# Kernel tuning notes

Measured on AMD Instinct MI355X. Metric: run time of the kernel, lower is better.

## Reference

```python
import jax, jax.numpy as jnp
import numpy as np

N_NODES = 500_000
N_EDGES = 16_000_000


def _gcn_conv(x, src, dst, deg_inv_sqrt, W, b, n):
    # PyG GCNConv: linear transform, then symmetric-normalized aggregation
    h = x @ W                                   # [N, out]
    norm = deg_inv_sqrt[src] * deg_inv_sqrt[dst]  # [E+N]
    msgs = h[src] * norm[:, None]               # gather + scale, [E+N, out]
    out = jax.ops.segment_sum(msgs, dst, num_segments=n)  # scatter-add
    return out + b


def setup_inputs() -> dict:
    key = jax.random.key(0)
    k1, k2, k3, k4, k5, k6 = jax.random.split(key, 6)
    x = jax.random.normal(k1, (N_NODES, 12), dtype=jnp.float32)
    edge_index = jax.random.randint(k2, (2, N_EDGES), 0, N_NODES, dtype=jnp.int64)
    # glorot-style init for GCNConv weights, zero bias (PyG default)
    W1 = jax.random.normal(k3, (12, 16), dtype=jnp.float32) * (2.0 / (12 + 16)) ** 0.5
    b1 = jnp.zeros((16,), dtype=jnp.float32)
    W2 = jax.random.normal(k4, (16, 8), dtype=jnp.float32) * (2.0 / (16 + 8)) ** 0.5
    b2 = jnp.zeros((8,), dtype=jnp.float32)
    return {"x": x, "edge_index": edge_index, "W1": W1, "b1": b1, "W2": W2, "b2": b2}


def reference(x, edge_index, W1, b1, W2, b2):
    n = x.shape[0]
    # add self-loops (GCNConv default add_self_loops=True)
    loops = jnp.arange(n, dtype=edge_index.dtype)
    src = jnp.concatenate([edge_index[0], loops])
    dst = jnp.concatenate([edge_index[1], loops])
    # symmetric normalization: deg over destination including self-loops
    deg = jax.ops.segment_sum(jnp.ones_like(dst, dtype=x.dtype), dst, num_segments=n)
    deg_inv_sqrt = jnp.where(deg > 0, jax.lax.rsqrt(deg), 0.0)
    h = jax.nn.relu(_gcn_conv(x, src, dst, deg_inv_sqrt, W1, b1, n))
    out = _gcn_conv(h, src, dst, deg_inv_sqrt, W2, b2, n)
    return out
```

## Files before the change

### kernel.cpp

```cpp
#include <hip/hip_runtime.h>

#define TPB 512
#define SCH 8192
#define EPT 16
#define NPB 512
#define NBIN 1024
#define CAP 17408
#define KMAX 34
#define NCHK 16
#define SBIN (NPB * NCHK)
#define PAD1 17
#define PAD2 9

__device__ __forceinline__ unsigned int f2bf(float f) {
    unsigned int u = __float_as_uint(f);
    return (u + 0x7FFFu + ((u >> 16) & 1u)) >> 16;
}
__device__ __forceinline__ float4 bf4(uint2 q) {
    float4 r;
    r.x = __uint_as_float(q.x << 16);
    r.y = __uint_as_float(q.x & 0xFFFF0000u);
    r.z = __uint_as_float(q.y << 16);
    r.w = __uint_as_float(q.y & 0xFFFF0000u);
    return r;
}

__global__ void k_init(int* bcur, int B) {
    int i = blockIdx.x * blockDim.x + threadIdx.x;
    if (i < B) bcur[i] = i * CAP;
}

__global__ void k_scatter(const int* __restrict__ es, const int* __restrict__ ed,
                          int* bcur, int* __restrict__ epk, int E, int B) {
    __shared__ int pay[SCH];
    __shared__ int cnt[NBIN];
    __shared__ int sstart[NBIN + 1];
    __shared__ int gbase[NBIN];
    __shared__ int tsum[TPB];
    int t = threadIdx.x;
    int e0 = blockIdx.x * SCH;
    int m = min(E - e0, SCH);
    for (int i = t; i < NBIN; i += TPB) cnt[i] = 0;
    __syncthreads();
    int pk[EPT], rk[EPT];
#pragma unroll
    for (int k = 0; k < EPT; k++) {
        int i = t + k * TPB;
        if (i < m) {
            int s = es[e0 + i], d = ed[e0 + i];
            int b = d >> 9;
            int r = atomicAdd(&cnt[b], 1);
            rk[k] = (b << 14) | r;
            pk[k] = (s << 9) | (d & (NPB - 1));
        }
    }
    __syncthreads();
    int c0 = cnt[2 * t], c1 = cnt[2 * t + 1];
    tsum[t] = c0 + c1;
    __syncthreads();
    for (int off = 1; off < TPB; off <<= 1) {
        int u = (t >= off) ? tsum[t - off] : 0;
        __syncthreads();
        tsum[t] += u;
        __syncthreads();
    }
    int base = tsum[t] - c0 - c1;
    sstart[2 * t] = base;
    sstart[2 * t + 1] = base + c0;
    if (t == TPB - 1) sstart[NBIN] = tsum[t];
    gbase[2 * t]     = c0 ? atomicAdd(&bcur[2 * t], c0) : 0;
    gbase[2 * t + 1] = c1 ? atomicAdd(&bcur[2 * t + 1], c1) : 0;
    __syncthreads();
#pragma unroll
    for (int k = 0; k < EPT; k++) {
        int i = t + k * TPB;
        if (i < m) pay[sstart[rk[k] >> 14] + (rk[k] & 16383)] = pk[k];
    }
    __syncthreads();
    for (int i = t; i < m; i += TPB) {
        int lo = 0, hi = NBIN;
        while (hi - lo > 1) {
            int mid = (lo + hi) >> 1;
            if (sstart[mid] <= i) lo = mid; else hi = mid;
        }
        epk[gbase[lo] + (i - sstart[lo])] = pay[i];
    }
}

__global__ void k_prepsort(const float* __restrict__ x, const int* __restrict__ bcur,
                           int* epk, const float* __restrict__ W1,
                           float* __restrict__ dis, unsigned int* __restrict__ h0u,
                           int* __restrict__ rowptr, uint4* __restrict__ scnt, int n) {
    __shared__ int cnt[SBIN];
    __shared__ int tsum[TPB];
    __shared__ float sW1[192];
    int t = threadIdx.x;
    int b = blockIdx.x;
    if (t < 192) sW1[t] = W1[t];
    for (int i = t; i < SBIN; i += TPB) cnt[i] = 0;
    __syncthreads();
    int e0 = b * CAP, e1 = bcur[b];
    int p[KMAX];
#pragma unroll
    for (int k = 0; k < KMAX; k++) {
        int idx = e0 + t + k * TPB;
        if (idx < e1) {
            p[k] = epk[idx];
            int bin = ((p[k] & (NPB - 1)) << 4) | ((p[k] >> 24) & 15);
            atomicAdd(&cnt[bin], 1);
        }
    }
    __syncthreads();
    int deg = 0;
#pragma unroll
    for (int j = 0; j < 16; j++) deg += cnt[16 * t + j];
    tsum[t] = deg;
    __syncthreads();
    for (int off = 1; off < TPB; off <<= 1) {
        int u = (t >= off) ? tsum[t - off] : 0;
        __syncthreads();
        tsum[t] += u;
        __syncthreads();
    }
    int run = e0 + tsum[t] - deg;
    int base = b << 9;
    int v = base + t;
    if (v < n) rowptr[v] = run;
    unsigned int cw[4] = {0u, 0u, 0u, 0u};
#pragma unroll
    for (int j = 0; j < 16; j++) {
        int cj = cnt[16 * t + j];
        cnt[16 * t + j] = run;
        run += cj;
        cw[j >> 2] |= ((unsigned int)cj) << ((j & 3) * 8);
    }
    if (v < n) scnt[v] = make_uint4(cw[0], cw[1], cw[2], cw[3]);
    __syncthreads();
    unsigned short* eps = (unsigned short*)epk;
    size_t ebase = (size_t)b * CAP;
#pragma unroll
    for (int k = 0; k < KMAX; k++) {
        int idx = e0 + t + k * TPB;
        if (idx < e1) {
            int bin = ((p[k] & (NPB - 1)) << 4) | ((p[k] >> 24) & 15);
            int pos = atomicAdd(&cnt[bin], 1);
            eps[ebase + pos] = (unsigned short)((p[k] >> 9) & 32767);
        }
    }
    if (v < n) {
        float d = rsqrtf((float)(deg + 1));
        dis[v] = d;
        const float4* xp = (const float4*)(x + (size_t)v * 12);
        float4 a = xp[0], q = xp[1], cc = xp[2];
        float xi[12] = {a.x, a.y, a.z, a.w, q.x, q.y, q.z, q.w, cc.x, cc.y, cc.z, cc.w};
        float o[16];
#pragma unroll
        for (int j = 0; j < 16; j++) {
            float s = 0.f;
#pragma unroll
            for (int k = 0; k < 12; k++) s = fmaf(xi[k], sW1[k * 16 + j], s);
            o[j] = s * d;
        }
        unsigned int w[8];
#pragma unroll
        for (int j = 0; j < 8; j++)
            w[j] = f2bf(o[2 * j]) | (f2bf(o[2 * j + 1]) << 16);
        uint4* hp = (uint4*)(h0u + (size_t)v * 8);
        hp[0] = make_uint4(w[0], w[1], w[2], w[3]);
        hp[1] = make_uint4(w[4], w[5], w[6], w[7]);
    }
}

__global__ void k_agg1(const unsigned int* __restrict__ h0u, const float* __restrict__ dis,
                       const int* __restrict__ rowptr, const int* __restrict__ epk,
                       const unsigned char* __restrict__ scb,
                       const float* __restrict__ b1, const float* __restrict__ W2,
                       unsigned int* __restrict__ h2u, int n) {
    __shared__ float acc[NPB * PAD1];
    __shared__ float sb1[16], sW2[128];
    int t = threadIdx.x;
    int b = blockIdx.x;
    if (t < 128) sW2[t] = W2[t];
    else if (t < 144) sb1[t - 128] = b1[t - 128];
    const unsigned short* eps = ((const unsigned short*)epk) + (size_t)b * CAP;
    const uint2* h0v = (const uint2*)h0u;
    int base = b << 9;
    int nn = min(NPB, n - base);
    int g = t >> 2, m = t & 3;
    float4 a[4];
    int cur[4];
#pragma unroll
    for (int u = 0; u < 4; u++) {
        int vl = 4 * g + u;
        if (vl < nn) {
            int v = base + vl;
            cur[u] = rowptr[v];
            a[u] = bf4(h0v[(size_t)v * 4 + m]);
        } else {
            cur[u] = 0;
            a[u] = make_float4(0.f, 0.f, 0.f, 0.f);
        }
    }
    for (int c = 0; c < NCHK; c++) {
        int cb = c << 15;
#pragma unroll
        for (int u = 0; u < 4; u++) {
            int vl = 4 * g + u;
            if (vl < nn) {
                int cnt = scb[(size_t)(base + vl) * NCHK + c];
                int end = cur[u] + cnt;
                int j = cur[u];
                cur[u] = end;
                for (; j + 1 < end; j += 2) {
                    int s0 = cb | eps[j], s1 = cb | eps[j + 1];
                    float4 q0 = bf4(h0v[(size_t)s0 * 4 + m]);
                    float4 q1 = bf4(h0v[(size_t)s1 * 4 + m]);
                    a[u].x += q0.x + q1.x; a[u].y += q0.y + q1.y;
                    a[u].z += q0.z + q1.z; a[u].w += q0.w + q1.w;
                }
                if (j < end) {
                    int s0 = cb | eps[j];
                    float4 q0 = bf4(h0v[(size_t)s0 * 4 + m]);
                    a[u].x += q0.x; a[u].y += q0.y; a[u].z += q0.z; a[u].w += q0.w;
                }
            }
        }
        __syncthreads();
    }
#pragma unroll
    for (int u = 0; u < 4; u++) {
        int vl = 4 * g + u;
        if (vl < nn) {
            float* ar = acc + vl * PAD1 + 4 * m;
            ar[0] = a[u].x; ar[1] = a[u].y; ar[2] = a[u].z; ar[3] = a[u].w;
        }
    }
    __syncthreads();
    if (t < nn) {
        int v = base + t;
        float dv = dis[v];
        float* ar = acc + t * PAD1;
        float h1[16];
#pragma unroll
        for (int j = 0; j < 16; j++)
            h1[j] = fmaxf(fmaf(dv, ar[j], sb1[j]), 0.f);
        float o[8];
#pragma unroll
        for (int j = 0; j < 8; j++) {
            float s = 0.f;
#pragma unroll
            for (int k = 0; k < 16; k++) s = fmaf(h1[k], sW2[k * 8 + j], s);
            o[j] = s * dv;
        }
        unsigned int w[4];
#pragma unroll
        for (int j = 0; j < 4; j++)
            w[j] = f2bf(o[2 * j]) | (f2bf(o[2 * j + 1]) << 16);
        ((uint4*)h2u)[v] = make_uint4(w[0], w[1], w[2], w[3]);
    }
}

__global__ void k_agg2(const unsigned int* __restrict__ h2u, const float* __restrict__ dis,
                       const int* __restrict__ rowptr, const int* __restrict__ epk,
                       const unsigned char* __restrict__ scb,
                       const float* __restrict__ b2, float* __restrict__ out, int n) {
    __shared__ float acc[NPB * PAD2];
    __shared__ float sb2[8];
    int t = threadIdx.x;
    int b = blockIdx.x;
    if (t < 8) sb2[t] = b2[t];
    const unsigned short* eps = ((const unsigned short*)epk) + (size_t)b * CAP;
    const uint2* h2v = (const uint2*)h2u;
    int base = b << 9;
    int nn = min(NPB, n - base);
    int g = t >> 1, m = t & 1;
    float4 a[2];
    int cur[2];
#pragma unroll
    for (int u = 0; u < 2; u++) {
        int vl = 2 * g + u;
        if (vl < nn) {
            int v = base + vl;
            cur[u] = rowptr[v];
            a[u] = bf4(h2v[(size_t)v * 2 + m]);
        } else {
            cur[u] = 0;
            a[u] = make_float4(0.f, 0.f, 0.f, 0.f);
        }
    }
    for (int c = 0; c < NCHK; c++) {
        int cb = c << 15;
#pragma unroll
        for (int u = 0; u < 2; u++) {
            int vl = 2 * g + u;
            if (vl < nn) {
                int cnt = scb[(size_t)(base + vl) * NCHK + c];
                int end = cur[u] + cnt;
                int j = cur[u];
                cur[u] = end;
                for (; j + 1 < end; j += 2) {
                    int s0 = cb | eps[j], s1 = cb | eps[j + 1];
                    float4 q0 = bf4(h2v[(size_t)s0 * 2 + m]);
                    float4 q1 = bf4(h2v[(size_t)s1 * 2 + m]);
                    a[u].x += q0.x + q1.x; a[u].y += q0.y + q1.y;
                    a[u].z += q0.z + q1.z; a[u].w += q0.w + q1.w;
                }
                if (j < end) {
                    int s0 = cb | eps[j];
                    float4 q0 = bf4(h2v[(size_t)s0 * 2 + m]);
                    a[u].x += q0.x; a[u].y += q0.y; a[u].z += q0.z; a[u].w += q0.w;
                }
            }
        }
        __syncthreads();
    }
#pragma unroll
    for (int u = 0; u < 2; u++) {
        int vl = 2 * g + u;
        if (vl < nn) {
            float* ar = acc + vl * PAD2 + 4 * m;
            ar[0] = a[u].x; ar[1] = a[u].y; ar[2] = a[u].z; ar[3] = a[u].w;
        }
    }
    __syncthreads();
    if (t < nn) {
        int v = base + t;
        float dv = dis[v];
        float* ar = acc + t * PAD2;
        float4* op = (float4*)(out + (size_t)v * 8);
        op[0] = make_float4(fmaf(dv, ar[0], sb2[0]), fmaf(dv, ar[1], sb2[1]),
                            fmaf(dv, ar[2], sb2[2]), fmaf(dv, ar[3], sb2[3]));
        op[1] = make_float4(fmaf(dv, ar[4], sb2[4]), fmaf(dv, ar[5], sb2[5]),
                            fmaf(dv, ar[6], sb2[6]), fmaf(dv, ar[7], sb2[7]));
    }
}

extern "C" void kernel_launch(void* const* d_in, const int* in_sizes, int n_in,
                              void* d_out, int out_size, void* d_ws, size_t ws_size,
                              hipStream_t stream) {
    const float* x  = (const float*)d_in[0];
    const int*   ei = (const int*)d_in[1];
    const float* W1 = (const float*)d_in[2];
    const float* b1 = (const float*)d_in[3];
    const float* W2 = (const float*)d_in[4];
    const float* b2 = (const float*)d_in[5];
    float* out = (float*)d_out;

    int n = in_sizes[0] / 12;
    int E = in_sizes[1] / 2;
    const int* es = ei;
    const int* ed = ei + E;

    int B = (n + NPB - 1) >> 9;

    char* wp = (char*)d_ws;
    int* bcur  = (int*)wp;
    int* rowptr = (int*)(wp + (16 << 10));
    size_t nAl = ((size_t)n + 15) & ~(size_t)15;
    float* dis = (float*)(rowptr + nAl + 16);
    unsigned int* h0u = (unsigned int*)(dis + nAl);
    unsigned int* h2u = h0u + 8 * nAl;
    int* epk   = (int*)(h2u + 4 * nAl);
    uint4* scnt = (uint4*)(epk + (size_t)B * CAP);

    int nchunks = (E + SCH - 1) / SCH;

    k_init<<<(B + 255) / 256, 256, 0, stream>>>(bcur, B);
    k_scatter<<<nchunks, TPB, 0, stream>>>(es, ed, bcur, epk, E, B);
    k_prepsort<<<B, TPB, 0, stream>>>(x, bcur, epk, W1, dis, h0u, rowptr, scnt, n);
    k_agg1<<<B, TPB, 0, stream>>>(h0u, dis, rowptr, epk, (const unsigned char*)scnt, b1, W2, h2u, n);
    k_agg2<<<B, TPB, 0, stream>>>(h2u, dis, rowptr, epk, (const unsigned char*)scnt, b2, out, n);
}
```

Before: 913.7 us.

## Replace chunk-synchronized aggregation with per-node edge loops using per-edge chunk ids

Drops the 16-chunk sweep with block barriers in both aggregation kernels. Each node now walks its whole edge list once, rebuilding the full source index from a new per-edge byte array holding the chunk id. The per-node chunk-count table is replaced by a 16-bit degree array. Gathers are widened to 16-byte loads, with fewer threads per node (2 in layer 1, 1 in layer 2), and k_agg2 no longer stages through shared memory. This removes barriers and per-chunk bookkeeping. In exchange it adds an extra byte of traffic per edge and gives up the chunk-ordered gather locality that kept source rows within a small cache window.

```diff
diff --git a/kernel.cpp b/kernel.cpp
--- a/kernel.cpp
+++ b/kernel.cpp
@@ -10,18 +10,17 @@
 #define NCHK 16
 #define SBIN (NPB * NCHK)
 #define PAD1 17
-#define PAD2 9
 
 __device__ __forceinline__ unsigned int f2bf(float f) {
     unsigned int u = __float_as_uint(f);
     return (u + 0x7FFFu + ((u >> 16) & 1u)) >> 16;
 }
-__device__ __forceinline__ float4 bf4(uint2 q) {
+__device__ __forceinline__ float4 bf4(unsigned int a, unsigned int b) {
     float4 r;
-    r.x = __uint_as_float(q.x << 16);
-    r.y = __uint_as_float(q.x & 0xFFFF0000u);
-    r.z = __uint_as_float(q.y << 16);
-    r.w = __uint_as_float(q.y & 0xFFFF0000u);
+    r.x = __uint_as_float(a << 16);
+    r.y = __uint_as_float(a & 0xFFFF0000u);
+    r.z = __uint_as_float(b << 16);
+    r.w = __uint_as_float(b & 0xFFFF0000u);
     return r;
 }
 
@@ -88,9 +87,10 @@
 }
 
 __global__ void k_prepsort(const float* __restrict__ x, const int* __restrict__ bcur,
-                           int* epk, const float* __restrict__ W1,
+                           int* epk, unsigned char* __restrict__ cid,
+                           const float* __restrict__ W1,
                            float* __restrict__ dis, unsigned int* __restrict__ h0u,
-                           int* __restrict__ rowptr, uint4* __restrict__ scnt, int n) {
+                           int* __restrict__ rowptr, unsigned short* __restrict__ degs, int n) {
     __shared__ int cnt[SBIN];
     __shared__ int tsum[TPB];
     __shared__ float sW1[192];
@@ -125,16 +125,13 @@
     int run = e0 + tsum[t] - deg;
     int base = b << 9;
     int v = base + t;
-    if (v < n) rowptr[v] = run;
-    unsigned int cw[4] = {0u, 0u, 0u, 0u};
+    if (v < n) { rowptr[v] = run; degs[v] = (unsigned short)deg; }
 #pragma unroll
     for (int j = 0; j < 16; j++) {
         int cj = cnt[16 * t + j];
         cnt[16 * t + j] = run;
         run += cj;
-        cw[j >> 2] |= ((unsigned int)cj) << ((j & 3) * 8);
-    }
-    if (v < n) scnt[v] = make_uint4(cw[0], cw[1], cw[2], cw[3]);
+    }
     __syncthreads();
     unsigned short* eps = (unsigned short*)epk;
     size_t ebase = (size_t)b * CAP;
@@ -145,6 +142,7 @@
             int bin = ((p[k] & (NPB - 1)) << 4) | ((p[k] >> 24) & 15);
             int pos = atomicAdd(&cnt[bin], 1);
             eps[ebase + pos] = (unsigned short)((p[k] >> 9) & 32767);
+            cid[pos] = (unsigned char)((p[k] >> 24) & 15);
         }
     }
     if (v < n) {
@@ -172,8 +170,8 @@
 }
 
 __global__ void k_agg1(const unsigned int* __restrict__ h0u, const float* __restrict__ dis,
-                       const int* __restrict__ rowptr, const int* __restrict__ epk,
-                       const unsigned char* __restrict__ scb,
+                       const int* __restrict__ rowptr, const unsigned short* __restrict__ degs,
+                       const int* __restrict__ epk, const unsigned char* __restrict__ cid,
                        const float* __restrict__ b1, const float* __restrict__ W2,
                        unsigned int* __restrict__ h2u, int n) {
     __shared__ float acc[NPB * PAD1];
@@ -183,56 +181,44 @@
     if (t < 128) sW2[t] = W2[t];
     else if (t < 144) sb1[t - 128] = b1[t - 128];
     const unsigned short* eps = ((const unsigned short*)epk) + (size_t)b * CAP;
-    const uint2* h0v = (const uint2*)h0u;
+    const uint4* h0q = (const uint4*)h0u;
     int base = b << 9;
     int nn = min(NPB, n - base);
-    int g = t >> 2, m = t & 3;
-    float4 a[4];
-    int cur[4];
-#pragma unroll
-    for (int u = 0; u < 4; u++) {
-        int vl = 4 * g + u;
+    int g = t >> 1, m = t & 1;
+#pragma unroll
+    for (int u = 0; u < 2; u++) {
+        int vl = 2 * g + u;
+        float4 aLo = make_float4(0.f, 0.f, 0.f, 0.f);
+        float4 aHi = make_float4(0.f, 0.f, 0.f, 0.f);
         if (vl < nn) {
             int v = base + vl;
-            cur[u] = rowptr[v];
-            a[u] = bf4(h0v[(size_t)v * 4 + m]);
-        } else {
-            cur[u] = 0;
-            a[u] = make_float4(0.f, 0.f, 0.f, 0.f);
-        }
-    }
-    for (int c = 0; c < NCHK; c++) {
-        int cb = c << 15;
-#pragma unroll
-        for (int u = 0; u < 4; u++) {
-            int vl = 4 * g + u;
-            if (vl < nn) {
-                int cnt = scb[(size_t)(base + vl) * NCHK + c];
-                int end = cur[u] + cnt;
-                int j = cur[u];
-                cur[u] = end;
-                for (; j + 1 < end; j += 2) {
-                    int s0 = cb | eps[j], s1 = cb | eps[j + 1];
-                    float4 q0 = bf4(h0v[(size_t)s0 * 4 + m]);
-                    float4 q1 = bf4(h0v[(size_t)s1 * 4 + m]);
-                    a[u].x += q0.x + q1.x; a[u].y += q0.y + q1.y;
-                    a[u].z += q0.z + q1.z; a[u].w += q0.w + q1.w;
-                }
-                if (j < end) {
-                    int s0 = cb | eps[j];
-                    float4 q0 = bf4(h0v[(size_t)s0 * 4 + m]);
-                    a[u].x += q0.x; a[u].y += q0.y; a[u].z += q0.z; a[u].w += q0.w;
-                }
+            uint4 qs = h0q[(size_t)v * 2 + m];
+            aLo = bf4(qs.x, qs.y);
+            aHi = bf4(qs.z, qs.w);
+            int j = rowptr[v];
+            int end = j + degs[v];
+            for (; j + 1 < end; j += 2) {
+                int s0 = (cid[j] << 15) | eps[j];
+                int s1 = (cid[j + 1] << 15) | eps[j + 1];
+                uint4 q0 = h0q[(size_t)s0 * 2 + m];
+                uint4 q1 = h0q[(size_t)s1 * 2 + m];
+                float4 f0 = bf4(q0.x, q0.y), g0 = bf4(q0.z, q0.w);
+                float4 f1 = bf4(q1.x, q1.y), g1 = bf4(q1.z, q1.w);
+                aLo.x += f0.x + f1.x; aLo.y += f0.y + f1.y;
+                aLo.z += f0.z + f1.z; aLo.w += f0.w + f1.w;
+                aHi.x += g0.x + g1.x; aHi.y += g0.y + g1.y;
+                aHi.z += g0.z + g1.z; aHi.w += g0.w + g1.w;
             }
-        }
-        __syncthreads();
-    }
-#pragma unroll
-    for (int u = 0; u < 4; u++) {
-        int vl = 4 * g + u;
-        if (vl < nn) {
-            float* ar = acc + vl * PAD1 + 4 * m;
-            ar[0] = a[u].x; ar[1] = a[u].y; ar[2] = a[u].z; ar[3] = a[u].w;
+            if (j < end) {
+                int s0 = (cid[j] << 15) | eps[j];
+                uint4 q0 = h0q[(size_t)s0 * 2 + m];
+                float4 f0 = bf4(q0.x, q0.y), g0 = bf4(q0.z, q0.w);
+                aLo.x += f0.x; aLo.y += f0.y; aLo.z += f0.z; aLo.w += f0.w;
+                aHi.x += g0.x; aHi.y += g0.y; aHi.z += g0.z; aHi.w += g0.w;
+            }
+            float* ar = acc + vl * PAD1 + 8 * m;
+            ar[0] = aLo.x; ar[1] = aLo.y; ar[2] = aLo.z; ar[3] = aLo.w;
+            ar[4] = aHi.x; ar[5] = aHi.y; ar[6] = aHi.z; ar[7] = aHi.w;
         }
     }
     __syncthreads();
@@ -261,78 +247,45 @@
 }
 
 __global__ void k_agg2(const unsigned int* __restrict__ h2u, const float* __restrict__ dis,
-                       const int* __restrict__ rowptr, const int* __restrict__ epk,
-                       const unsigned char* __restrict__ scb,
+                       const int* __restrict__ rowptr, const unsigned short* __restrict__ degs,
+                       const int* __restrict__ epk, const unsigned char* __restrict__ cid,
                        const float* __restrict__ b2, float* __restrict__ out, int n) {
-    __shared__ float acc[NPB * PAD2];
-    __shared__ float sb2[8];
     int t = threadIdx.x;
     int b = blockIdx.x;
-    if (t < 8) sb2[t] = b2[t];
     const unsigned short* eps = ((const unsigned short*)epk) + (size_t)b * CAP;
-    const uint2* h2v = (const uint2*)h2u;
-    int base = b << 9;
-    int nn = min(NPB, n - base);
-    int g = t >> 1, m = t & 1;
-    float4 a[2];
-    int cur[2];
-#pragma unroll
-    for (int u = 0; u < 2; u++) {
-        int vl = 2 * g + u;
-        if (vl < nn) {
-            int v = base + vl;
-            cur[u] = rowptr[v];
-            a[u] = bf4(h2v[(size_t)v * 2 + m]);
-        } else {
-            cur[u] = 0;
-            a[u] = make_float4(0.f, 0.f, 0.f, 0.f);
-        }
-    }
-    for (int c = 0; c < NCHK; c++) {
-        int cb = c << 15;
-#pragma unroll
-        for (int u = 0; u < 2; u++) {
-            int vl = 2 * g + u;
-            if (vl < nn) {
-                int cnt = scb[(size_t)(base + vl) * NCHK + c];
-                int end = cur[u] + cnt;
-                int j = cur[u];
-                cur[u] = end;
-                for (; j + 1 < end; j += 2) {
-                    int s0 = cb | eps[j], s1 = cb | eps[j + 1];
-                    float4 q0 = bf4(h2v[(size_t)s0 * 2 + m]);
-                    float4 q1 = bf4(h2v[(size_t)s1 * 2 + m]);
-                    a[u].x += q0.x + q1.x; a[u].y += q0.y + q1.y;
-                    a[u].z += q0.z + q1.z; a[u].w += q0.w + q1.w;
-                }
-                if (j < end) {
-                    int s0 = cb | eps[j];
-                    float4 q0 = bf4(h2v[(size_t)s0 * 2 + m]);
-                    a[u].x += q0.x; a[u].y += q0.y; a[u].z += q0.z; a[u].w += q0.w;
-                }
-            }
-        }
-        __syncthreads();
-    }
-#pragma unroll
-    for (int u = 0; u < 2; u++) {
-        int vl = 2 * g + u;
-        if (vl < nn) {
-            float* ar = acc + vl * PAD2 + 4 * m;
-            ar[0] = a[u].x; ar[1] = a[u].y; ar[2] = a[u].z; ar[3] = a[u].w;
-        }
-    }
-    __syncthreads();
-    if (t < nn) {
-        int v = base + t;
-        float dv = dis[v];
-        float* ar = acc + t * PAD2;
-        float4* op = (float4*)(out + (size_t)v * 8);
-        op[0] = make_float4(fmaf(dv, ar[0], sb2[0]), fmaf(dv, ar[1], sb2[1]),
-                            fmaf(dv, ar[2], sb2[2]), fmaf(dv, ar[3], sb2[3]));
-        op[1] = make_float4(fmaf(dv, ar[4], sb2[4]), fmaf(dv, ar[5], sb2[5]),
-                            fmaf(dv, ar[6], sb2[6]), fmaf(dv, ar[7], sb2[7]));
-    }
+    const uint4* h2q = (const uint4*)h2u;
+    int v = (b << 9) + t;
+    if (v >= n) return;
+    uint4 qs = h2q[v];
+    float4 aLo = bf4(qs.x, qs.y);
+    float4 aHi = bf4(qs.z, qs.w);
+    int j = rowptr[v];
+    int end = j + degs[v];
+    for (; j + 1 < end; j += 2) {
+        int s0 = (cid[j] << 15) | eps[j];
+        int s1 = (cid[j + 1] << 15) | eps[j + 1];
+        uint4 q0 = h2q[s0];
+        uint4 q1 = h2q[s1];
+        float4 f0 = bf4(q0.x, q0.y), g0 = bf4(q0.z, q0.w);
+        float4 f1 = bf4(q1.x, q1.y), g1 = bf4(q1.z, q1.w);
+        aLo.x += f0.x + f1.x; aLo.y += f0.y + f1.y;
+        aLo.z += f0.z + f1.z; aLo.w += f0.w + f1.w;
+        aHi.x += g0.x + g1.x; aHi.y += g0.y + g1.y;
+        aHi.z += g0.z + g1.z; aHi.w += g0.w + g1.w;
+    }
+    if (j < end) {
+        int s0 = (cid[j] << 15) | eps[j];
+        uint4 q0 = h2q[s0];
+        float4 f0 = bf4(q0.x, q0.y), g0 = bf4(q0.z, q0.w);
+        aLo.x += f0.x; aLo.y += f0.y; aLo.z += f0.z; aLo.w += f0.w;
+        aHi.x += g0.x; aHi.y += g0.y; aHi.z += g0.z; aHi.w += g0.w;
+    }
+    float dv = dis[v];
+    float4* op = (float4*)(out + (size_t)v * 8);
+    op[0] = make_float4(fmaf(dv, aLo.x, b2[0]), fmaf(dv, aLo.y, b2[1]),
+                        fmaf(dv, aLo.z, b2[2]), fmaf(dv, aLo.w, b2[3]));
+    op[1] = make_float4(fmaf(dv, aHi.x, b2[4]), fmaf(dv, aHi.y, b2[5]),
+                        fmaf(dv, aHi.z, b2[6]), fmaf(dv, aHi.w, b2[7]));
 }
 
 extern "C" void kernel_launch(void* const* d_in, const int* in_sizes, int n_in,
@@ -358,16 +311,17 @@
     int* rowptr = (int*)(wp + (16 << 10));
     size_t nAl = ((size_t)n + 15) & ~(size_t)15;
     float* dis = (float*)(rowptr + nAl + 16);
-    unsigned int* h0u = (unsigned int*)(dis + nAl);
+    unsigned short* degs = (unsigned short*)(dis + nAl);
+    unsigned int* h0u = (unsigned int*)(degs + nAl);
     unsigned int* h2u = h0u + 8 * nAl;
     int* epk   = (int*)(h2u + 4 * nAl);
-    uint4* scnt = (uint4*)(epk + (size_t)B * CAP);
+    unsigned char* cid = (unsigned char*)(epk + (size_t)B * CAP);
 
     int nchunks = (E + SCH - 1) / SCH;
 
     k_init<<<(B + 255) / 256, 256, 0, stream>>>(bcur, B);
     k_scatter<<<nchunks, TPB, 0, stream>>>(es, ed, bcur, epk, E, B);
-    k_prepsort<<<B, TPB, 0, stream>>>(x, bcur, epk, W1, dis, h0u, rowptr, scnt, n);
-    k_agg1<<<B, TPB, 0, stream>>>(h0u, dis, rowptr, epk, (const unsigned char*)scnt, b1, W2, h2u, n);
-    k_agg2<<<B, TPB, 0, stream>>>(h2u, dis, rowptr, epk, (const unsigned char*)scnt, b2, out, n);
-}
+    k_prepsort<<<B, TPB, 0, stream>>>(x, bcur, epk, cid, W1, dis, h0u, rowptr, degs, n);
+    k_agg1<<<B, TPB, 0, stream>>>(h0u, dis, rowptr, degs, epk, cid, b1, W2, h2u, n);
+    k_agg2<<<B, TPB, 0, stream>>>(h2u, dis, rowptr, degs, epk, cid, b2, out, n);
+}
```

New measurement: 1.043 ms. 14.2% more time.
